# Optimization experiments

Hardware: AMD Instinct MI355X
Metric: run time of the kernel (lower is better)

The kernel has to match this reference:

```python
import jax, jax.numpy as jnp
import numpy as np
import math

ALGEBRA_DIM = 32

def _hadamard(n):
    H = np.array([[1.0]], dtype=np.float32)
    while H.shape[0] < n:
        H = np.block([[H, H], [H, -H]])
    return H

# Sylvester-ordered Hadamard matrix, normalized: equals the butterfly FHT with /sqrt(N)
H32 = jnp.asarray(_hadamard(ALGEBRA_DIM) / math.sqrt(ALGEBRA_DIM), dtype=jnp.float32)

def quantize_ternary(w):
    # BitNet-b1.58 style absmean ternary quantization with straight-through estimator
    scale = jnp.mean(jnp.abs(w)) + 1e-8
    w_q = jnp.clip(jnp.round(w / scale), -1.0, 1.0) * scale
    return w + jax.lax.stop_gradient(w_q - w)

def setup_inputs() -> dict:
    key = jax.random.key(0)
    k1, k2, k3 = jax.random.split(key, 3)
    B, T = 4, 2048
    in_o = out_o = 128  # in_features = out_features = 4096
    x = jax.random.normal(k1, (B, T, ALGEBRA_DIM * in_o), dtype=jnp.float32)
    weight = jax.random.uniform(k2, (ALGEBRA_DIM, out_o, in_o), dtype=jnp.float32) * 2.0 - 1.0
    alpha = jnp.ones((ALGEBRA_DIM, in_o), dtype=jnp.float32)
    beta_init = math.sqrt(3.0 / (2.0 * in_o))
    beta = jnp.ones((ALGEBRA_DIM, out_o), dtype=jnp.float32) * beta_init
    return {"x": x, "weight": weight, "alpha": alpha, "beta": beta}

def reference(x, weight, alpha, beta):
    B, T, D = x.shape
    G = ALGEBRA_DIM
    in_o = D // G
    w_q = quantize_ternary(weight)                      # [G, out_o, in_o]
    xp = x.reshape(B, T, G, in_o) * alpha               # [B,T,G,in_o]
    # FHT over algebra dim G (Sylvester WHT, /sqrt(G) folded into H32)
    xm = jnp.einsum('btgi,gh->bthi', xp, H32)           # [B,T,G,in_o]
    # grouped ternary matmul: btgi,gio->btgo with w_q transposed
    yp = jnp.einsum('bthi,hoi->btho', xm, w_q)          # [B,T,G,out_o]
    ym = jnp.einsum('btho,hg->btgo', yp, H32)           # FHT over algebra dim again
    y = ym * beta                                       # [B,T,G,out_o]
    return y.reshape(B, T, -1)
```

## Files before the change

kernel.cpp:

```cpp
#include <hip/hip_runtime.h>
#include <cstdint>
#include <cstddef>

#define TM 16
#define IP 136
#define SLAB (TM * IP)

__device__ __forceinline__ unsigned short f2bf(float f) {
  union { float f; unsigned int u; } c; c.f = f;
  unsigned int u = c.u;
  return (unsigned short)((u + 0x7FFFu + ((u >> 16) & 1u)) >> 16);
}
__device__ __forceinline__ float bf2f(unsigned short h) {
  union { unsigned int u; float f; } c; c.u = ((unsigned int)h) << 16; return c.f;
}

__device__ __forceinline__ void fht32(float* v) {
  #pragma unroll
  for (int s = 1; s < 32; s <<= 1) {
    #pragma unroll
    for (int a = 0; a < 32; ++a) {
      if ((a & s) == 0) {
        float u0 = v[a], u1 = v[a + s];
        v[a] = u0 + u1;
        v[a + s] = u0 - u1;
      }
    }
  }
}

typedef __attribute__((ext_vector_type(8))) short bf16x8;
typedef __attribute__((ext_vector_type(4))) float f32x4;
typedef __attribute__((ext_vector_type(2))) float f32x2;

__global__ void kred1(const float* __restrict__ w, double* __restrict__ partials) {
  const int tid = threadIdx.x;
  const int base = blockIdx.x * 2048 + tid;
  double s = 0.0;
  #pragma unroll
  for (int j = 0; j < 8; ++j) s += (double)fabsf(w[base + j * 256]);
  #pragma unroll
  for (int off = 32; off > 0; off >>= 1) s += __shfl_down(s, off, 64);
  __shared__ double sh[4];
  if ((tid & 63) == 0) sh[tid >> 6] = s;
  __syncthreads();
  if (tid == 0) partials[blockIdx.x] = sh[0] + sh[1] + sh[2] + sh[3];
}

__global__ void kprep(const float* __restrict__ w, const double* __restrict__ partials,
                      float* __restrict__ scale_out, unsigned short* __restrict__ wqt) {
  const int tid = threadIdx.x;
  __shared__ float s_sc;
  if (tid < 64) {
    double s = partials[tid] + partials[tid + 64] + partials[tid + 128] + partials[tid + 192];
    #pragma unroll
    for (int off = 32; off > 0; off >>= 1) s += __shfl_down(s, off, 64);
    if (tid == 0) s_sc = (float)(s / 524288.0) + 1e-8f;
  }
  __syncthreads();
  const float sc = s_sc;
  if (blockIdx.x == 0 && tid == 0) scale_out[0] = sc;
  const int cid = blockIdx.x * 256 + tid;
  const int lane = cid & 63, ks = (cid >> 6) & 3, nt = (cid >> 8) & 7, h = cid >> 11;
  const int m = lane & 15, quad = lane >> 4;
  const float* src = w + h * 16384 + (nt * 16 + m) * 128 + ks * 32 + quad * 8;
  bf16x8 vv;
  #pragma unroll
  for (int j = 0; j < 8; ++j) {
    float q = rintf(src[j] / sc);
    q = fminf(1.f, fmaxf(-1.f, q));
    vv[j] = (short)f2bf(q);
  }
  *(bf16x8*)(wqt + (size_t)cid * 8) = vv;
}

__global__ __launch_bounds__(1024)
__attribute__((amdgpu_waves_per_eu(4, 4)))
void had_main(
    const float* __restrict__ x,
    const unsigned short* __restrict__ wqt,
    const float* __restrict__ alpha,
    const float* __restrict__ beta,
    const float* __restrict__ scale_p,
    float* __restrict__ y) {
  extern __shared__ unsigned short lds[];
  const int tid = threadIdx.x;
  const long tok0 = (long)blockIdx.x * TM;
  const int t  = tid >> 6;
  const int ih = (tid & 63) << 1;

  {
    const float* xrow = x + (size_t)(tok0 + t) * 4096 + ih;
    float va[32], vb[32];
    #pragma unroll
    for (int g = 0; g < 32; ++g) {
      f32x2 v = *(const f32x2*)(xrow + (size_t)g * 128);
      va[g] = v[0]; vb[g] = v[1];
    }
    #pragma unroll
    for (int g = 0; g < 32; ++g) {
      f32x2 a = *(const f32x2*)(alpha + g * 128 + ih);
      va[g] *= a[0]; vb[g] *= a[1];
    }
    fht32(va);
    fht32(vb);
    #pragma unroll
    for (int h = 0; h < 32; ++h) {
      unsigned int pk = (unsigned int)f2bf(va[h]) | ((unsigned int)f2bf(vb[h]) << 16);
      *(unsigned int*)(lds + (h * TM + t) * IP + ih) = pk;
    }
  }
  __syncthreads();

  {
    const int wave = tid >> 6;
    const int lane = tid & 63;
    const int m = lane & 15;
    const int quad = lane >> 4;
    unsigned short* slab0 = lds + (wave)      * SLAB;
    unsigned short* slab1 = lds + (wave + 16) * SLAB;
    const unsigned short* wh0 = wqt + (size_t)(wave)      * 16384 + (size_t)lane * 8;
    const unsigned short* wh1 = wqt + (size_t)(wave + 16) * 16384 + (size_t)lane * 8;

    bf16x8 af[4];
    bf16x8 b0[4], b1[4], b2[4];
    #pragma unroll
    for (int ks = 0; ks < 4; ++ks) b0[ks] = *(const bf16x8*)(wh0 + (size_t)ks * 512);
    #pragma unroll
    for (int ks = 0; ks < 4; ++ks) b1[ks] = *(const bf16x8*)(wh0 + (size_t)(4 + ks) * 512);
    #pragma unroll
    for (int ks = 0; ks < 4; ++ks)
      af[ks] = *(const bf16x8*)(slab0 + m * IP + ks * 32 + quad * 8);

    #pragma unroll
    for (int nt = 0; nt < 8; ++nt) {
      {
        const unsigned short* wsrc = (nt < 6) ? (wh0 + (size_t)((nt + 2) * 4) * 512)
                                              : (wh1 + (size_t)((nt - 6) * 4) * 512);
        #pragma unroll
        for (int ks = 0; ks < 4; ++ks) b2[ks] = *(const bf16x8*)(wsrc + (size_t)ks * 512);
      }
      f32x4 acc = {0.f, 0.f, 0.f, 0.f};
      #pragma unroll
      for (int ks = 0; ks < 4; ++ks)
        acc = __builtin_amdgcn_mfma_f32_16x16x32_bf16(af[ks], b0[ks], acc, 0, 0, 0);
      #pragma unroll
      for (int r = 0; r < 4; ++r)
        slab0[(quad * 4 + r) * IP + nt * 16 + m] = f2bf(acc[r]);
      #pragma unroll
      for (int ks = 0; ks < 4; ++ks) { b0[ks] = b1[ks]; b1[ks] = b2[ks]; }
    }

    #pragma unroll
    for (int ks = 0; ks < 4; ++ks)
      af[ks] = *(const bf16x8*)(slab1 + m * IP + ks * 32 + quad * 8);

    #pragma unroll
    for (int nt = 0; nt < 8; ++nt) {
      if (nt < 6) {
        const unsigned short* wsrc = wh1 + (size_t)((nt + 2) * 4) * 512;
        #pragma unroll
        for (int ks = 0; ks < 4; ++ks) b2[ks] = *(const bf16x8*)(wsrc + (size_t)ks * 512);
      }
      f32x4 acc = {0.f, 0.f, 0.f, 0.f};
      #pragma unroll
      for (int ks = 0; ks < 4; ++ks)
        acc = __builtin_amdgcn_mfma_f32_16x16x32_bf16(af[ks], b0[ks], acc, 0, 0, 0);
      #pragma unroll
      for (int r = 0; r < 4; ++r)
        slab1[(quad * 4 + r) * IP + nt * 16 + m] = f2bf(acc[r]);
      #pragma unroll
      for (int ks = 0; ks < 4; ++ks) { b0[ks] = b1[ks]; b1[ks] = b2[ks]; }
    }
  }
  __syncthreads();

  {
    const float sc32 = scale_p[0] * (1.0f / 32.0f);
    float v0[32], v1[32];
    #pragma unroll
    for (int h = 0; h < 32; ++h) {
      unsigned int pk = *(const unsigned int*)(lds + (h * TM + t) * IP + ih);
      v0[h] = bf2f((unsigned short)(pk & 0xFFFFu));
      v1[h] = bf2f((unsigned short)(pk >> 16));
    }
    fht32(v0);
    fht32(v1);
    float* yrow = y + (size_t)(tok0 + t) * 4096 + ih;
    #pragma unroll
    for (int g = 0; g < 32; ++g) {
      f32x2 b = *(const f32x2*)(beta + g * 128 + ih);
      const float c0 = b[0] * sc32;
      const float c1 = b[1] * sc32;
      f32x2 o; o[0] = v0[g] * c0; o[1] = v1[g] * c1;
      *(f32x2*)(yrow + (size_t)g * 128) = o;
    }
  }
}

extern "C" void kernel_launch(void* const* d_in, const int* in_sizes, int n_in,
                              void* d_out, int out_size, void* d_ws, size_t ws_size,
                              hipStream_t stream) {
  (void)in_sizes; (void)n_in; (void)out_size; (void)ws_size;
  const float* x     = (const float*)d_in[0];
  const float* w     = (const float*)d_in[1];
  const float* alpha = (const float*)d_in[2];
  const float* beta  = (const float*)d_in[3];
  float* y = (float*)d_out;

  char* ws = (char*)d_ws;
  unsigned short* wqt = (unsigned short*)(ws);
  float* scale     = (float*)(ws + 1048576);
  double* partials = (double*)(ws + 1048584);

  (void)hipFuncSetAttribute(reinterpret_cast<const void*>(had_main),
                            hipFuncAttributeMaxDynamicSharedMemorySize, 139264);

  hipLaunchKernelGGL(kred1,    dim3(256), dim3(256),  0,      stream, w, partials);
  hipLaunchKernelGGL(kprep,    dim3(256), dim3(256),  0,      stream, w, partials, scale, wqt);
  hipLaunchKernelGGL(had_main, dim3(512), dim3(1024), 139264, stream, x, wqt, alpha, beta, scale, y);
}
```

Before: 281.0 us.

## Process columns in two scalar passes and shrink weight prefetch to one stage

The FHT load and store phases now handle one column per pass, two passes in sequence, instead of two interleaved columns with float2 vector accesses. This halves the live register arrays. The weight prefetch in the MFMA loop goes from a two-deep to a one-deep register pipeline, and the waves_per_eu attribute is replaced with launch_bounds(1024,1). The aim is lower register pressure to avoid spills, traded for narrower scalar global accesses, 16-bit LDS writes, and less latency hiding on the weight loads.

```diff
diff --git a/kernel.cpp b/kernel.cpp
--- a/kernel.cpp
+++ b/kernel.cpp
@@ -31,7 +31,6 @@
 
 typedef __attribute__((ext_vector_type(8))) short bf16x8;
 typedef __attribute__((ext_vector_type(4))) float f32x4;
-typedef __attribute__((ext_vector_type(2))) float f32x2;
 
 __global__ void kred1(const float* __restrict__ w, double* __restrict__ partials) {
   const int tid = threadIdx.x;
@@ -74,8 +73,7 @@
   *(bf16x8*)(wqt + (size_t)cid * 8) = vv;
 }
 
-__global__ __launch_bounds__(1024)
-__attribute__((amdgpu_waves_per_eu(4, 4)))
+__global__ __launch_bounds__(1024, 1)
 void had_main(
     const float* __restrict__ x,
     const unsigned short* __restrict__ wqt,
@@ -87,28 +85,20 @@
   const int tid = threadIdx.x;
   const long tok0 = (long)blockIdx.x * TM;
   const int t  = tid >> 6;
-  const int ih = (tid & 63) << 1;
-
-  {
-    const float* xrow = x + (size_t)(tok0 + t) * 4096 + ih;
-    float va[32], vb[32];
-    #pragma unroll
-    for (int g = 0; g < 32; ++g) {
-      f32x2 v = *(const f32x2*)(xrow + (size_t)g * 128);
-      va[g] = v[0]; vb[g] = v[1];
-    }
-    #pragma unroll
-    for (int g = 0; g < 32; ++g) {
-      f32x2 a = *(const f32x2*)(alpha + g * 128 + ih);
-      va[g] *= a[0]; vb[g] *= a[1];
-    }
-    fht32(va);
-    fht32(vb);
-    #pragma unroll
-    for (int h = 0; h < 32; ++h) {
-      unsigned int pk = (unsigned int)f2bf(va[h]) | ((unsigned int)f2bf(vb[h]) << 16);
-      *(unsigned int*)(lds + (h * TM + t) * IP + ih) = pk;
-    }
+  const int il = tid & 63;
+
+  #pragma unroll
+  for (int p = 0; p < 2; ++p) {
+    const int i = il + p * 64;
+    const float* xrow = x + (size_t)(tok0 + t) * 4096 + i;
+    float v[32];
+    #pragma unroll
+    for (int g = 0; g < 32; ++g) v[g] = xrow[(size_t)g * 128];
+    #pragma unroll
+    for (int g = 0; g < 32; ++g) v[g] *= alpha[g * 128 + i];
+    fht32(v);
+    #pragma unroll
+    for (int h = 0; h < 32; ++h) lds[(h * TM + t) * IP + i] = f2bf(v[h]);
   }
   __syncthreads();
 
@@ -122,12 +112,9 @@
     const unsigned short* wh0 = wqt + (size_t)(wave)      * 16384 + (size_t)lane * 8;
     const unsigned short* wh1 = wqt + (size_t)(wave + 16) * 16384 + (size_t)lane * 8;
 
-    bf16x8 af[4];
-    bf16x8 b0[4], b1[4], b2[4];
-    #pragma unroll
-    for (int ks = 0; ks < 4; ++ks) b0[ks] = *(const bf16x8*)(wh0 + (size_t)ks * 512);
-    #pragma unroll
-    for (int ks = 0; ks < 4; ++ks) b1[ks] = *(const bf16x8*)(wh0 + (size_t)(4 + ks) * 512);
+    bf16x8 af[4], cur[4], nxt[4];
+    #pragma unroll
+    for (int ks = 0; ks < 4; ++ks) cur[ks] = *(const bf16x8*)(wh0 + (size_t)ks * 512);
     #pragma unroll
     for (int ks = 0; ks < 4; ++ks)
       af[ks] = *(const bf16x8*)(slab0 + m * IP + ks * 32 + quad * 8);
@@ -135,20 +122,19 @@
     #pragma unroll
     for (int nt = 0; nt < 8; ++nt) {
       {
-        const unsigned short* wsrc = (nt < 6) ? (wh0 + (size_t)((nt + 2) * 4) * 512)
-                                              : (wh1 + (size_t)((nt - 6) * 4) * 512);
+        const unsigned short* wsrc = (nt < 7) ? (wh0 + (size_t)((nt + 1) * 4) * 512) : wh1;
         #pragma unroll
-        for (int ks = 0; ks < 4; ++ks) b2[ks] = *(const bf16x8*)(wsrc + (size_t)ks * 512);
+        for (int ks = 0; ks < 4; ++ks) nxt[ks] = *(const bf16x8*)(wsrc + (size_t)ks * 512);
       }
       f32x4 acc = {0.f, 0.f, 0.f, 0.f};
       #pragma unroll
       for (int ks = 0; ks < 4; ++ks)
-        acc = __builtin_amdgcn_mfma_f32_16x16x32_bf16(af[ks], b0[ks], acc, 0, 0, 0);
+        acc = __builtin_amdgcn_mfma_f32_16x16x32_bf16(af[ks], cur[ks], acc, 0, 0, 0);
       #pragma unroll
       for (int r = 0; r < 4; ++r)
         slab0[(quad * 4 + r) * IP + nt * 16 + m] = f2bf(acc[r]);
       #pragma unroll
-      for (int ks = 0; ks < 4; ++ks) { b0[ks] = b1[ks]; b1[ks] = b2[ks]; }
+      for (int ks = 0; ks < 4; ++ks) cur[ks] = nxt[ks];
     }
 
     #pragma unroll
@@ -157,43 +143,37 @@
 
     #pragma unroll
     for (int nt = 0; nt < 8; ++nt) {
-      if (nt < 6) {
-        const unsigned short* wsrc = wh1 + (size_t)((nt + 2) * 4) * 512;
+      if (nt < 7) {
+        const unsigned short* wsrc = wh1 + (size_t)((nt + 1) * 4) * 512;
         #pragma unroll
-        for (int ks = 0; ks < 4; ++ks) b2[ks] = *(const bf16x8*)(wsrc + (size_t)ks * 512);
+        for (int ks = 0; ks < 4; ++ks) nxt[ks] = *(const bf16x8*)(wsrc + (size_t)ks * 512);
       }
       f32x4 acc = {0.f, 0.f, 0.f, 0.f};
       #pragma unroll
       for (int ks = 0; ks < 4; ++ks)
-        acc = __builtin_amdgcn_mfma_f32_16x16x32_bf16(af[ks], b0[ks], acc, 0, 0, 0);
+        acc = __builtin_amdgcn_mfma_f32_16x16x32_bf16(af[ks], cur[ks], acc, 0, 0, 0);
       #pragma unroll
       for (int r = 0; r < 4; ++r)
         slab1[(quad * 4 + r) * IP + nt * 16 + m] = f2bf(acc[r]);
       #pragma unroll
-      for (int ks = 0; ks < 4; ++ks) { b0[ks] = b1[ks]; b1[ks] = b2[ks]; }
+      for (int ks = 0; ks < 4; ++ks) cur[ks] = nxt[ks];
     }
   }
   __syncthreads();
 
   {
     const float sc32 = scale_p[0] * (1.0f / 32.0f);
-    float v0[32], v1[32];
-    #pragma unroll
-    for (int h = 0; h < 32; ++h) {
-      unsigned int pk = *(const unsigned int*)(lds + (h * TM + t) * IP + ih);
-      v0[h] = bf2f((unsigned short)(pk & 0xFFFFu));
-      v1[h] = bf2f((unsigned short)(pk >> 16));
-    }
-    fht32(v0);
-    fht32(v1);
-    float* yrow = y + (size_t)(tok0 + t) * 4096 + ih;
-    #pragma unroll
-    for (int g = 0; g < 32; ++g) {
-      f32x2 b = *(const f32x2*)(beta + g * 128 + ih);
-      const float c0 = b[0] * sc32;
-      const float c1 = b[1] * sc32;
-      f32x2 o; o[0] = v0[g] * c0; o[1] = v1[g] * c1;
-      *(f32x2*)(yrow + (size_t)g * 128) = o;
+    #pragma unroll
+    for (int p = 0; p < 2; ++p) {
+      const int i = il + p * 64;
+      float v[32];
+      #pragma unroll
+      for (int h = 0; h < 32; ++h) v[h] = bf2f(lds[(h * TM + t) * IP + i]);
+      fht32(v);
+      float* yrow = y + (size_t)(tok0 + t) * 4096 + i;
+      #pragma unroll
+      for (int g = 0; g < 32; ++g)
+        yrow[(size_t)g * 128] = v[g] * (beta[g * 128 + i] * sc32);
     }
   }
 }
```

New measurement: 299.2 us. 1.06x slower.
